# Kernel tuning notes

Measured on AMD Instinct MI355X. Metric: run time of the kernel, lower is better.

Reference implementation:

```python
import jax, jax.numpy as jnp
import numpy as np

N, D, K = 8192, 64, 32

def setup_inputs() -> dict:
    key = jax.random.key(0)
    anchor_x = jax.random.normal(key, (N, D), dtype=jnp.float32)
    return {"anchor_x": anchor_x, "k": K}

def reference(anchor_x, k):
    """Equivalent of NNUtil_GPVAE.build_sequential_nn_idx with faiss/IndexFlatL2.
    For each row r in [k, N), find the k nearest (squared-L2) neighbors among
    rows [0, r) of anchor_x. Returns (sq_dists [N-k, k] ascending, idx [N-k, k]).
    """
    n = anchor_x.shape[0]
    q = anchor_x[k:]                                   # [N-k, D] queries
    sq = jnp.sum(anchor_x * anchor_x, axis=-1)         # [N]
    # squared L2: ||q||^2 + ||x||^2 - 2 q.x  -> [N-k, N]
    dist = sq[k:, None] + sq[None, :] - 2.0 * (q @ anchor_x.T)
    dist = jnp.maximum(dist, 0.0)
    # causal mask: row r may only see database entries j < r (growing index)
    r = jnp.arange(k, n, dtype=jnp.int32)[:, None]     # [N-k, 1]
    j = jnp.arange(n, dtype=jnp.int32)[None, :]        # [1, N]
    dist = jnp.where(j < r, dist, jnp.inf)
    neg_d, idx = jax.lax.top_k(-dist, k)               # ascending distances
    return -neg_d, idx.astype(jnp.int64)
```

## Files before the change

kernel.cpp:

```cpp
#include <hip/hip_runtime.h>
#include <math.h>

#define NROWS 8192
#define DIM   64
#define KSEL  32
#define NQ    (NROWS - KSEL)
#define P1LEN 512
#define CAP   1024
#define FILT_CB 256
#define NMASK (NROWS / 16)

typedef __attribute__((ext_vector_type(8))) short bf16x8;
typedef __attribute__((ext_vector_type(4))) float f32x4;

__global__ void norms_kernel(const float* __restrict__ x, float* __restrict__ sq) {
    int j = blockIdx.x * blockDim.x + threadIdx.x;
    if (j >= NROWS) return;
    const float* xr = x + (size_t)j * DIM;
    float r[8];
#pragma unroll
    for (int u = 0; u < 8; ++u) r[u] = 0.0f;
#pragma unroll
    for (int i = 0; i < DIM; i += 8) {
#pragma unroll
        for (int u = 0; u < 8; ++u)
            r[u] = __fmaf_rn(xr[i + u], xr[i + u], r[u]);
    }
    const float s04 = __fadd_rn(r[0], r[4]);
    const float s26 = __fadd_rn(r[2], r[6]);
    const float s15 = __fadd_rn(r[1], r[5]);
    const float s37 = __fadd_rn(r[3], r[7]);
    sq[j] = __fadd_rn(__fadd_rn(s04, s26), __fadd_rn(s15, s37));
}

__global__ __launch_bounds__(256)
void transpose_kernel(const float* __restrict__ x, float* __restrict__ xT) {
    __shared__ float tile[64][65];
    const int jb  = blockIdx.x * 64;
    const int t   = threadIdx.x;
    const int row = t >> 2;
    const int cb  = (t & 3) * 16;
    const float4* src = reinterpret_cast<const float4*>(
        x + (size_t)(jb + row) * DIM + cb);
#pragma unroll
    for (int i = 0; i < 4; ++i) {
        const float4 v = src[i];
        tile[row][cb + 4 * i + 0] = v.x; tile[row][cb + 4 * i + 1] = v.y;
        tile[row][cb + 4 * i + 2] = v.z; tile[row][cb + 4 * i + 3] = v.w;
    }
    __syncthreads();
    const int k = row;
#pragma unroll
    for (int i = 0; i < 4; ++i) {
        float4 w;
        w.x = tile[cb + 4 * i + 0][k]; w.y = tile[cb + 4 * i + 1][k];
        w.z = tile[cb + 4 * i + 2][k]; w.w = tile[cb + 4 * i + 3][k];
        *reinterpret_cast<float4*>(xT + (size_t)k * NROWS + jb + cb + 4 * i) = w;
    }
}

__global__ __launch_bounds__(256)
void convert_kernel(const float* __restrict__ x, unsigned short* __restrict__ xb) {
    const int i = (blockIdx.x * blockDim.x + threadIdx.x) * 4;
    if (i >= NROWS * DIM) return;
    const float4 v = *reinterpret_cast<const float4*>(x + i);
    const float vv[4] = {v.x, v.y, v.z, v.w};
    unsigned short o[4];
#pragma unroll
    for (int u = 0; u < 4; ++u) {
        const unsigned b = __float_as_uint(vv[u]);
        o[u] = (unsigned short)((b + 0x7FFFu + ((b >> 16) & 1u)) >> 16);
    }
    *reinterpret_cast<ushort4*>(xb + i) = make_ushort4(o[0], o[1], o[2], o[3]);
}

__global__ __launch_bounds__(256)
void pass1_kernel(const float* __restrict__ x, const float* __restrict__ xT,
                  const float* __restrict__ sq,
                  unsigned long long* __restrict__ tau0,
                  unsigned int* __restrict__ cnt,
                  unsigned long long* __restrict__ lists) {
    const int wave = threadIdx.x >> 6;
    const int lane = threadIdx.x & 63;
    const int qi   = blockIdx.x * 4 + wave;
    const int r    = qi + KSEL;
    const int P    = min(r, P1LEN);

    const float* qp  = x + (size_t)r * DIM;
    const float  sqr = sq[r];

    float acc[8];
#pragma unroll
    for (int u = 0; u < 8; ++u) acc[u] = 0.0f;
    const float4* xT4 = reinterpret_cast<const float4*>(xT);
#pragma unroll 4
    for (int k = 0; k < DIM; ++k) {
        const float  qk = qp[k];
        const float4 c0 = xT4[(size_t)k * (NROWS / 4) + lane];
        const float4 c1 = xT4[(size_t)k * (NROWS / 4) + 64 + lane];
        acc[0] = __fmaf_rn(qk, c0.x, acc[0]);
        acc[1] = __fmaf_rn(qk, c0.y, acc[1]);
        acc[2] = __fmaf_rn(qk, c0.z, acc[2]);
        acc[3] = __fmaf_rn(qk, c0.w, acc[3]);
        acc[4] = __fmaf_rn(qk, c1.x, acc[4]);
        acc[5] = __fmaf_rn(qk, c1.y, acc[5]);
        acc[6] = __fmaf_rn(qk, c1.z, acc[6]);
        acc[7] = __fmaf_rn(qk, c1.w, acc[7]);
    }

    unsigned long long key[8];
    {
        const float4 sq0 = *reinterpret_cast<const float4*>(sq + 4 * lane);
        const float4 sq1 = *reinterpret_cast<const float4*>(sq + 256 + 4 * lane);
        const float sqc[8] = {sq0.x, sq0.y, sq0.z, sq0.w,
                              sq1.x, sq1.y, sq1.z, sq1.w};
#pragma unroll
        for (int u = 0; u < 8; ++u) {
            const int j = (u < 4) ? (4 * lane + u) : (256 + 4 * lane + (u - 4));
            const float dd = fmaxf(
                __fsub_rn(__fadd_rn(sqr, sqc[u]), __fmul_rn(2.0f, acc[u])), 0.0f);
            key[u] = (j < P)
                ? (((unsigned long long)__float_as_uint(dd) << 32) | (unsigned)j)
                : ~0ull;
        }
    }

    unsigned long long pmin = ~0ull;
#pragma unroll
    for (int s = 0; s < 8; ++s) pmin = key[s] < pmin ? key[s] : pmin;

    unsigned long long g = ~0ull;
    for (int it = 0; it < KSEL; ++it) {
        unsigned long long v = pmin;
#pragma unroll
        for (int off = 32; off > 0; off >>= 1) {
            const unsigned long long o = __shfl_down(v, off, 64);
            v = o < v ? o : v;
        }
        g = __shfl(v, 0, 64);
        if (lane == 0) lists[(size_t)qi * CAP + it] = g;
        if (pmin == g) {
#pragma unroll
            for (int s = 0; s < 8; ++s) if (key[s] == g) key[s] = ~0ull;
            pmin = ~0ull;
#pragma unroll
            for (int s = 0; s < 8; ++s) pmin = key[s] < pmin ? key[s] : pmin;
        }
    }
    if (lane == 0) { tau0[qi] = g; cnt[qi] = KSEL; }
}

__global__ __launch_bounds__(256)
void filter_kernel(const unsigned short* __restrict__ xb,
                   const float* __restrict__ sq,
                   const unsigned long long* __restrict__ tau0,
                   unsigned short* __restrict__ bm) {
    const int qb   = blockIdx.x;
    const int jb   = P1LEN + blockIdx.y * FILT_CB;
    const int r_hi = min(KSEL + (qb + 1) * 64, NROWS);
    if (jb >= r_hi) return;

    const int wave = threadIdx.x >> 6;
    const int lane = threadIdx.x & 63;
    const int rb   = KSEL + qb * 64 + wave * 16;
    const int col  = lane & 15;
    const int kg   = lane >> 4;

    const int arow = min(rb + col, NROWS - 1);
    const bf16x8 a0 = *reinterpret_cast<const bf16x8*>(xb + (size_t)arow * DIM + kg * 8);
    const bf16x8 a1 = *reinterpret_cast<const bf16x8*>(xb + (size_t)arow * DIM + 32 + kg * 8);

    float sqr[4], thm[4]; int rr[4];
#pragma unroll
    for (int i = 0; i < 4; ++i) {
        const int r = rb + kg * 4 + i;
        rr[i]  = r;
        const int rc = min(r, NROWS - 1);
        sqr[i] = sq[rc];
        thm[i] = (r < NROWS) ? __uint_as_float((unsigned)(tau0[r - KSEL] >> 32))
                             : -1.0f;
    }

    for (int sub = 0; sub < FILT_CB / 16; ++sub) {
        const int j0 = jb + sub * 16;
        if (j0 >= r_hi) break;
        const int j  = j0 + col;
        const int jc = min(j, NROWS - 1);
        const bf16x8 b0 = *reinterpret_cast<const bf16x8*>(xb + (size_t)jc * DIM + kg * 8);
        const bf16x8 b1 = *reinterpret_cast<const bf16x8*>(xb + (size_t)jc * DIM + 32 + kg * 8);
        f32x4 acc = {0.f, 0.f, 0.f, 0.f};
        acc = __builtin_amdgcn_mfma_f32_16x16x32_bf16(a0, b0, acc, 0, 0, 0);
        acc = __builtin_amdgcn_mfma_f32_16x16x32_bf16(a1, b1, acc, 0, 0, 0);
        const float sqc = sq[jc];
#pragma unroll
        for (int i = 0; i < 4; ++i) {
            const float s = __fadd_rn(sqr[i], sqc);
            const float d = __fmaf_rn(-2.0f, acc[i], s);
            const bool accept = (j < rr[i]) &&
                                (d <= __fmaf_rn(0.01171875f, s, thm[i]));
            const unsigned long long mask = __ballot(accept);
            const unsigned slice = (unsigned)((mask >> (kg * 16)) & 0xFFFFull);
            if (col == 0 && rr[i] < NROWS)
                bm[(size_t)rr[i] * NMASK + (j0 >> 4)] = (unsigned short)slice;
        }
    }
}

__global__ __launch_bounds__(256)
void refine_kernel(const float* __restrict__ x, const float* __restrict__ sq,
                   const unsigned long long* __restrict__ tau0,
                   const unsigned short* __restrict__ bm,
                   unsigned int* __restrict__ cnt,
                   unsigned long long* __restrict__ lists) {
    __shared__ unsigned lcnt;
    const int qi = blockIdx.x;
    const int r  = qi + KSEL;
    if (threadIdx.x == 0) lcnt = KSEL;
    __syncthreads();

    const unsigned th = (unsigned)(tau0[qi] >> 32);
    const float* qp = x + (size_t)r * DIM;
    const float  sqr = sq[r];
    unsigned long long* dst = lists + (size_t)qi * CAP;
    const int mlast = (r - 1) >> 4;

    for (int m = (P1LEN / 16) + (int)threadIdx.x; m <= mlast; m += 256) {
        unsigned msk = bm[(size_t)r * NMASK + m];
        while (msk) {
            const int b = __builtin_ctz(msk);
            msk &= msk - 1;
            const int j = (m << 4) + b;
            const float4* cp4 = reinterpret_cast<const float4*>(x + (size_t)j * DIM);
            float4 c[16];
#pragma unroll
            for (int k = 0; k < 16; ++k) c[k] = cp4[k];
            float acc = 0.0f;
#pragma unroll
            for (int k = 0; k < 16; ++k) {
                acc = __fmaf_rn(qp[4 * k + 0], c[k].x, acc);
                acc = __fmaf_rn(qp[4 * k + 1], c[k].y, acc);
                acc = __fmaf_rn(qp[4 * k + 2], c[k].z, acc);
                acc = __fmaf_rn(qp[4 * k + 3], c[k].w, acc);
            }
            const float dd = fmaxf(
                __fsub_rn(__fadd_rn(sqr, sq[j]), __fmul_rn(2.0f, acc)), 0.0f);
            const unsigned bits = __float_as_uint(dd);
            if (bits <= th) {
                const unsigned slot = atomicAdd(&lcnt, 1u);
                if (slot < CAP)
                    dst[slot] = ((unsigned long long)bits << 32) | (unsigned)j;
            }
        }
    }
    __syncthreads();
    if (threadIdx.x == 0) cnt[qi] = min(lcnt, (unsigned)CAP);
}

__global__ __launch_bounds__(64)
void merge_kernel(const unsigned long long* __restrict__ lists,
                  const unsigned int* __restrict__ cnt,
                  float* __restrict__ out_d, float* __restrict__ out_i) {
    const int qi   = blockIdx.x;
    const int lane = threadIdx.x;
    const int ne   = min((int)cnt[qi], CAP);
    const unsigned long long* src = lists + (size_t)qi * CAP;

    unsigned long long k[16];
#pragma unroll
    for (int s = 0; s < 16; ++s) {
        const int idx = lane + (s << 6);
        k[s] = (idx < ne) ? src[idx] : ~0ull;
    }
    unsigned long long pmin = ~0ull;
#pragma unroll
    for (int s = 0; s < 16; ++s) pmin = k[s] < pmin ? k[s] : pmin;

    for (int it = 0; it < KSEL; ++it) {
        unsigned long long v = pmin;
#pragma unroll
        for (int off = 32; off > 0; off >>= 1) {
            const unsigned long long o = __shfl_down(v, off, 64);
            v = o < v ? o : v;
        }
        const unsigned long long g = __shfl(v, 0, 64);
        if (lane == 0) {
            out_d[(size_t)qi * KSEL + it] = __uint_as_float((unsigned)(g >> 32));
            out_i[(size_t)qi * KSEL + it] = (float)(unsigned)(g & 0xFFFFFFFFu);
        }
        if (pmin == g) {
#pragma unroll
            for (int s = 0; s < 16; ++s) if (k[s] == g) k[s] = ~0ull;
            pmin = ~0ull;
#pragma unroll
            for (int s = 0; s < 16; ++s) pmin = k[s] < pmin ? k[s] : pmin;
        }
    }
}

extern "C" void kernel_launch(void* const* d_in, const int* in_sizes, int n_in,
                              void* d_out, int out_size, void* d_ws, size_t ws_size,
                              hipStream_t stream) {
    const float* x = (const float*)d_in[0];
    float* sq = (float*)d_ws;
    unsigned long long* tau0 =
        (unsigned long long*)((char*)d_ws + 32768);
    unsigned int* cnt = (unsigned int*)((char*)d_ws + 98304);
    unsigned long long* lists =
        (unsigned long long*)((char*)d_ws + 131072);
    unsigned short* xb =
        (unsigned short*)((char*)d_ws + 66977792);
    float* xT = (float*)((char*)d_ws + 68026368);
    unsigned short* bm =
        (unsigned short*)((char*)d_ws + 70123520);
    float* out_d = (float*)d_out;
    float* out_i = out_d + (size_t)NQ * KSEL;

    norms_kernel<<<NROWS / 256, 256, 0, stream>>>(x, sq);
    transpose_kernel<<<NROWS / 64, 256, 0, stream>>>(x, xT);
    convert_kernel<<<NROWS * DIM / 1024, 256, 0, stream>>>(x, xb);
    pass1_kernel<<<NQ / 4, 256, 0, stream>>>(x, xT, sq, tau0, cnt, lists);
    dim3 gf(128, (NROWS - P1LEN) / FILT_CB);
    filter_kernel<<<gf, 256, 0, stream>>>(xb, sq, tau0, bm);
    refine_kernel<<<NQ, 256, 0, stream>>>(x, sq, tau0, bm, cnt, lists);
    merge_kernel<<<NQ, 64, 0, stream>>>(lists, cnt, out_d, out_i);
}
```

Measured before the change: 335.1 us.

## Fuse refine and merge kernels with shared-memory candidate list

```diff
diff --git a/kernel.cpp b/kernel.cpp
--- a/kernel.cpp
+++ b/kernel.cpp
@@ -78,7 +78,6 @@
 void pass1_kernel(const float* __restrict__ x, const float* __restrict__ xT,
                   const float* __restrict__ sq,
                   unsigned long long* __restrict__ tau0,
-                  unsigned int* __restrict__ cnt,
                   unsigned long long* __restrict__ lists) {
     const int wave = threadIdx.x >> 6;
     const int lane = threadIdx.x & 63;
@@ -147,7 +146,7 @@
             for (int s = 0; s < 8; ++s) pmin = key[s] < pmin ? key[s] : pmin;
         }
     }
-    if (lane == 0) { tau0[qi] = g; cnt[qi] = KSEL; }
+    if (lane == 0) tau0[qi] = g;
 }
 
 __global__ __launch_bounds__(256)
@@ -207,24 +206,26 @@
 }
 
 __global__ __launch_bounds__(256)
-void refine_kernel(const float* __restrict__ x, const float* __restrict__ sq,
-                   const unsigned long long* __restrict__ tau0,
-                   const unsigned short* __restrict__ bm,
-                   unsigned int* __restrict__ cnt,
-                   unsigned long long* __restrict__ lists) {
+void refine_merge_kernel(const float* __restrict__ x, const float* __restrict__ sq,
+                         const unsigned long long* __restrict__ tau0,
+                         const unsigned short* __restrict__ bm,
+                         const unsigned long long* __restrict__ lists,
+                         float* __restrict__ out_d, float* __restrict__ out_i) {
+    __shared__ unsigned long long keys[CAP];
     __shared__ unsigned lcnt;
-    const int qi = blockIdx.x;
-    const int r  = qi + KSEL;
-    if (threadIdx.x == 0) lcnt = KSEL;
+    const int qi  = blockIdx.x;
+    const int r   = qi + KSEL;
+    const int tid = threadIdx.x;
+    if (tid == 0) lcnt = KSEL;
+    if (tid < KSEL) keys[tid] = lists[(size_t)qi * CAP + tid];
     __syncthreads();
 
     const unsigned th = (unsigned)(tau0[qi] >> 32);
     const float* qp = x + (size_t)r * DIM;
     const float  sqr = sq[r];
-    unsigned long long* dst = lists + (size_t)qi * CAP;
     const int mlast = (r - 1) >> 4;
 
-    for (int m = (P1LEN / 16) + (int)threadIdx.x; m <= mlast; m += 256) {
+    for (int m = (P1LEN / 16) + tid; m <= mlast; m += 256) {
         unsigned msk = bm[(size_t)r * NMASK + m];
         while (msk) {
             const int b = __builtin_ctz(msk);
@@ -248,28 +249,21 @@
             if (bits <= th) {
                 const unsigned slot = atomicAdd(&lcnt, 1u);
                 if (slot < CAP)
-                    dst[slot] = ((unsigned long long)bits << 32) | (unsigned)j;
+                    keys[slot] = ((unsigned long long)bits << 32) | (unsigned)j;
             }
         }
     }
     __syncthreads();
-    if (threadIdx.x == 0) cnt[qi] = min(lcnt, (unsigned)CAP);
-}
-
-__global__ __launch_bounds__(64)
-void merge_kernel(const unsigned long long* __restrict__ lists,
-                  const unsigned int* __restrict__ cnt,
-                  float* __restrict__ out_d, float* __restrict__ out_i) {
-    const int qi   = blockIdx.x;
-    const int lane = threadIdx.x;
-    const int ne   = min((int)cnt[qi], CAP);
-    const unsigned long long* src = lists + (size_t)qi * CAP;
+
+    if (tid >= 64) return;
+    const int lane = tid;
+    const int ne   = min((int)lcnt, CAP);
 
     unsigned long long k[16];
 #pragma unroll
     for (int s = 0; s < 16; ++s) {
         const int idx = lane + (s << 6);
-        k[s] = (idx < ne) ? src[idx] : ~0ull;
+        k[s] = (idx < ne) ? keys[idx] : ~0ull;
     }
     unsigned long long pmin = ~0ull;
 #pragma unroll
@@ -304,7 +298,6 @@
     float* sq = (float*)d_ws;
     unsigned long long* tau0 =
         (unsigned long long*)((char*)d_ws + 32768);
-    unsigned int* cnt = (unsigned int*)((char*)d_ws + 98304);
     unsigned long long* lists =
         (unsigned long long*)((char*)d_ws + 131072);
     unsigned short* xb =
@@ -318,9 +311,9 @@
     norms_kernel<<<NROWS / 256, 256, 0, stream>>>(x, sq);
     transpose_kernel<<<NROWS / 64, 256, 0, stream>>>(x, xT);
     convert_kernel<<<NROWS * DIM / 1024, 256, 0, stream>>>(x, xb);
-    pass1_kernel<<<NQ / 4, 256, 0, stream>>>(x, xT, sq, tau0, cnt, lists);
+    pass1_kernel<<<NQ / 4, 256, 0, stream>>>(x, xT, sq, tau0, lists);
     dim3 gf(128, (NROWS - P1LEN) / FILT_CB);
     filter_kernel<<<gf, 256, 0, stream>>>(xb, sq, tau0, bm);
-    refine_kernel<<<NQ, 256, 0, stream>>>(x, sq, tau0, bm, cnt, lists);
-    merge_kernel<<<NQ, 64, 0, stream>>>(lists, cnt, out_d, out_i);
-}
+    refine_merge_kernel<<<NQ, 256, 0, stream>>>(x, sq, tau0, bm, lists,
+                                                out_d, out_i);
+}
```

After: 304.8 us. -9.0%, faster.
